# Kernel tuning notes

Measured on AMD Instinct MI355X. Metric: run time of the kernel, lower is better.

The kernel has to match this reference:

```python
import jax, jax.numpy as jnp
import numpy as np

ALPHA = 0.5            # conf['alpha'] hybrid mixing
MAX_TOP_ANT = 50       # conf['max_top_antecedents']
MAX_SPAN_WIDTH = 30


def bucket_distance(d):
    # util.bucket_distance: identity 0..4, then log2 buckets, clipped to [0, 9]
    logspace = jnp.floor(jnp.log2(jnp.maximum(d, 1).astype(jnp.float32))).astype(d.dtype) + 3
    return jnp.clip(jnp.where(d <= 4, d, logspace), 0, 9)


def setup_inputs() -> dict:
    key = jax.random.key(0)
    ks = jax.random.split(key, 16)
    W, D, K, F, H = 4096, 768, 768, 20, 1000
    SPAN = 3 * D                      # span_emb_size = 3 * bert_emb_size
    PAIR = 3 * SPAN + F               # pair_emb_size (use_features only)
    std = 0.02

    mention_doc = jax.random.normal(ks[0], (W, D), jnp.float32)
    mention_doc_one = jax.random.normal(ks[1], (W, D), jnp.float32)
    top_span_starts = jnp.sort(jax.random.randint(ks[2], (K,), 0, W - MAX_SPAN_WIDTH))
    widths = jax.random.randint(ks[3], (K,), 0, MAX_SPAN_WIDTH)
    top_span_ends = jnp.minimum(top_span_starts + widths, W - 1)
    top_span_mention_scores = jax.random.normal(ks[4], (K,), jnp.float32)

    return {
        "mention_doc": mention_doc,
        "mention_doc_one": mention_doc_one,
        "top_span_starts": top_span_starts,
        "top_span_ends": top_span_ends,
        "top_span_mention_scores": top_span_mention_scores,
        # mention_token_attn: Linear(D -> 1)
        "attn_w": jax.random.normal(ks[5], (D,), jnp.float32) * std,
        "attn_b": jnp.zeros((), jnp.float32),
        # coarse_bilinear: Linear(SPAN -> SPAN)
        "coarse_w": jax.random.normal(ks[6], (SPAN, SPAN), jnp.float32) * std,
        "coarse_b": jnp.zeros((SPAN,), jnp.float32),
        # emb_antecedent_distance_prior [10, F] + antecedent_distance_score_ffnn Linear(F -> 1)
        "dist_prior_emb": jax.random.normal(ks[7], (10, F), jnp.float32) * std,
        "dist_w": jax.random.normal(ks[8], (F,), jnp.float32) * std,
        "dist_b": jnp.zeros((), jnp.float32),
        # emb_top_antecedent_distance [10, F]
        "top_dist_emb": jax.random.normal(ks[9], (10, F), jnp.float32) * std,
        # coref_score_ffnn: Linear(PAIR -> H), ReLU, Linear(H -> 1)
        "coref_w1": jax.random.normal(ks[10], (PAIR, H), jnp.float32) * std,
        "coref_b1": jnp.zeros((H,), jnp.float32),
        "coref_w2": jax.random.normal(ks[11], (H,), jnp.float32) * std,
        "coref_b2": jnp.zeros((), jnp.float32),
    }


def reference(mention_doc, mention_doc_one, top_span_starts, top_span_ends,
              top_span_mention_scores, attn_w, attn_b, coarse_w, coarse_b,
              dist_prior_emb, dist_w, dist_b, top_dist_emb,
              coref_w1, coref_b1, coref_w2, coref_b2):
    W = mention_doc.shape[0]
    K = top_span_starts.shape[0]
    C = min(K, MAX_TOP_ANT)
    NEG_INF = jnp.float32(-1e30) * 0 - jnp.inf  # true -inf, matches torch.log(0.)

    # --- span embeddings: start / end / head-attention over hybrid doc ---
    start_emb = mention_doc[top_span_starts]                      # [K, D]
    end_emb = mention_doc[top_span_ends]                          # [K, D]
    hybrid = mention_doc * (1.0 - ALPHA) + mention_doc_one * ALPHA
    token_attn = hybrid @ attn_w + attn_b                         # [W]
    tok = jnp.arange(W)
    span_tok_mask = (tok[None, :] >= top_span_starts[:, None]) & \
                    (tok[None, :] <= top_span_ends[:, None])      # [K, W]
    attn_raw = jnp.where(span_tok_mask, token_attn[None, :], NEG_INF)
    attn_probs = jax.nn.softmax(attn_raw, axis=1)                 # [K, W]
    head_emb = attn_probs @ hybrid                                # [K, D]
    span_emb = jnp.concatenate([start_emb, end_emb, head_emb], axis=1)  # [K, 3D]

    # --- coarse (fast) pairwise scores ---
    rng = jnp.arange(K)
    ant_offsets = rng[:, None] - rng[None, :]                     # [K, K]
    ant_mask = ant_offsets >= 1
    pair_sum = top_span_mention_scores[:, None] + top_span_mention_scores[None, :]
    src = span_emb @ coarse_w + coarse_b                          # coarse_bilinear
    fast = pair_sum + src @ span_emb.T
    fast = jnp.where(ant_mask, fast, NEG_INF)                     # + log(mask)
    dist_score = dist_prior_emb @ dist_w + dist_b                 # [10]
    fast = fast + dist_score[bucket_distance(ant_offsets)]        # distance prior

    # --- top-k antecedent pruning ---
    top_fast, top_idx = jax.lax.top_k(fast, C)                    # [K, C]
    top_ant_offsets = jnp.take_along_axis(ant_offsets, top_idx, axis=1)

    # --- fine-grained pairwise FFNN scoring ---
    dist_emb = top_dist_emb[bucket_distance(top_ant_offsets)]     # [K, C, F]
    ant_emb = span_emb[top_idx]                                   # [K, C, 3D]
    tgt_emb = jnp.broadcast_to(span_emb[:, None, :], ant_emb.shape)
    sim_emb = span_emb[:, None, :] * ant_emb
    pair_emb = jnp.concatenate([tgt_emb, ant_emb, sim_emb, dist_emb], axis=-1)  # [K, C, PAIR]
    h = jax.nn.relu(jnp.einsum('kcp,ph->kch', pair_emb, coref_w1) + coref_b1)
    slow = jnp.einsum('kch,h->kc', h, coref_w2) + coref_b2        # [K, C]
    top_scores = slow + top_fast

    # dummy antecedent (epsilon) column of zeros
    return jnp.concatenate([jnp.zeros((K, 1), top_scores.dtype), top_scores], axis=1)
```

## Files before the change

kernel.cpp:

```cpp
#include <hip/hip_runtime.h>
#include <math.h>

#define WTOK 4096
#define DD   768
#define KK   768
#define SPAN 2304
#define HH   1000
#define CC   50
#define NPAD 1024
#define NBIG 4352

typedef __attribute__((ext_vector_type(8))) short bf16x8;
typedef __attribute__((ext_vector_type(4))) float f32x4;
typedef unsigned short ushort;
typedef unsigned int uint;
typedef unsigned long long u64;

__device__ __forceinline__ int bucketd(int d) {
  int l = (d >= 1) ? (31 - __clz(d)) : 0;
  int v = (d <= 4) ? d : (l + 3);
  return min(max(v, 0), 9);
}
__device__ __forceinline__ ushort f2bf(float f) {
  uint u = __float_as_uint(f);
  return (ushort)((u + 0x7fffu + ((u >> 16) & 1u)) >> 16);
}
__device__ __forceinline__ uint pkmul_t(uint a, uint b) {
  float lo = __uint_as_float(a << 16) * __uint_as_float(b << 16);
  float hi = __uint_as_float(a & 0xffff0000u) * __uint_as_float(b & 0xffff0000u);
  return __builtin_amdgcn_perm(__float_as_uint(hi), __float_as_uint(lo), 0x07060302u);
}
__device__ __forceinline__ uint4 pkmul4(uint4 a, uint4 b) {
  uint4 r;
  r.x = pkmul_t(a.x, b.x); r.y = pkmul_t(a.y, b.y);
  r.z = pkmul_t(a.z, b.z); r.w = pkmul_t(a.w, b.w);
  return r;
}
__device__ __forceinline__ void dma16(const ushort* g, ushort* l) {
  __builtin_amdgcn_global_load_lds(
      (const __attribute__((address_space(1))) void*)g,
      (__attribute__((address_space(3))) void*)l, 16, 0, 0);
}
__device__ __forceinline__ u64 shflx64(u64 v, int msk) {
  uint lo = (uint)v, hi = (uint)(v >> 32);
  lo = (uint)__shfl_xor((int)lo, msk, 64);
  hi = (uint)__shfl_xor((int)hi, msk, 64);
  return ((u64)hi << 32) | lo;
}

#define PB_COARSE 5184
#define PB_W 2304
#define PB_SETUP_BASE (PB_COARSE + 3 * PB_W)
#define PB_SLOW_BASE  (PB_SETUP_BASE + 40)
#define PB_HYB_BASE   (PB_SLOW_BASE + 150)
#define PB_TOTAL      (PB_HYB_BASE + WTOK)

__global__ __launch_bounds__(256) void prep_k(
    const float* __restrict__ coarse_w, const float* __restrict__ W1,
    const float* __restrict__ dist_prior, const float* __restrict__ dist_w,
    const float* __restrict__ dist_b, const float* __restrict__ top_dist,
    const float* __restrict__ doc, const float* __restrict__ doc1,
    const float* __restrict__ attn_w, const float* __restrict__ attn_b,
    ushort* __restrict__ BigT, ushort* __restrict__ W1simT,
    float* __restrict__ dist_score, float* __restrict__ Pdist,
    float* __restrict__ slow, float* __restrict__ hybrid,
    float* __restrict__ tok_attn)
{
  int bid = blockIdx.x;
  int tid = threadIdx.x;
  if (bid >= PB_HYB_BASE) {
    int w = bid - PB_HYB_BASE;
    float part = 0.f;
    for (int d = tid; d < DD; d += 256) {
      float h = 0.5f * doc[(long)w * DD + d] + 0.5f * doc1[(long)w * DD + d];
      hybrid[(long)w * DD + d] = h;
      part += h * attn_w[d];
    }
    for (int off = 32; off > 0; off >>= 1) part += __shfl_down(part, off, 64);
    __shared__ float ws4[4];
    if ((tid & 63) == 0) ws4[tid >> 6] = part;
    __syncthreads();
    if (tid == 0) tok_attn[w] = ws4[0] + ws4[1] + ws4[2] + ws4[3] + attn_b[0];
    return;
  }
  if (bid >= PB_SLOW_BASE) {
    int t = (bid - PB_SLOW_BASE) * 256 + tid;
    if (t < KK * CC) slow[t] = 0.f;
    return;
  }
  if (bid >= PB_SETUP_BASE) {
    int t = (bid - PB_SETUP_BASE) * 256 + tid;
    if (t < 10) {
      float s = dist_b[0];
      for (int f = 0; f < 20; ++f) s += dist_prior[t * 20 + f] * dist_w[f];
      dist_score[t] = s;
    }
    if (t < 10 * HH) {
      int b = t / HH, h = t % HH;
      float s = 0.f;
      for (int f = 0; f < 20; ++f)
        s += top_dist[b * 20 + f] * W1[(long)(6912 + f) * HH + h];
      Pdist[t] = s;
    }
    return;
  }
  const float* in; int ldin, Cin, nbase, NBrows; ushort* out; int idx;
  int xt;
  if (bid < PB_COARSE) {
    idx = bid; in = coarse_w; ldin = SPAN; Cin = SPAN; nbase = 0;
    NBrows = NBIG; out = BigT; xt = SPAN / 32;
  } else {
    idx = bid - PB_COARSE;
    int region = idx / PB_W;
    idx = idx % PB_W;
    if (region == 0) { in = W1; nbase = 2304; NBrows = NBIG; out = BigT; }
    else if (region == 1) { in = W1 + (size_t)SPAN * HH; nbase = 3328; NBrows = NBIG; out = BigT; }
    else { in = W1 + (size_t)2 * SPAN * HH; nbase = 0; NBrows = NPAD; out = W1simT; }
    ldin = HH; Cin = HH; xt = NPAD / 32;
  }
  {
    int bx = idx % xt, by = idx / xt;
    __shared__ float tile[32][33];
    int n0 = bx * 32, p0 = by * 32;
    int tx = tid & 31, ty = tid >> 5;
    for (int i = ty; i < 32; i += 8) {
      int p = p0 + i, n = n0 + tx;
      tile[i][tx] = (n < Cin) ? in[(long)p * ldin + n] : 0.f;
    }
    __syncthreads();
    size_t slab = (size_t)(p0 >> 5) * NBrows * 32;
    for (int i = ty; i < 32; i += 8) {
      int n = n0 + i;
      out[slab + (size_t)(nbase + n) * 32 + tx] = f2bf(tile[tx][i]);
    }
  }
}

__global__ __launch_bounds__(256) void span_emb_k(
    const float* __restrict__ doc, const float* __restrict__ hybrid,
    const float* __restrict__ tok_attn, const int* __restrict__ starts,
    const int* __restrict__ ends, ushort* __restrict__ se_bf)
{
  int k = blockIdx.x;
  int s = starts[k], e = ends[k];
  int len = e - s + 1;
  int tid = threadIdx.x;
  __shared__ float p_s[32];
  if (tid < 32) {
    float v = (tid < len) ? tok_attn[s + tid] : -INFINITY;
    float m = v;
    for (int msk = 16; msk >= 1; msk >>= 1) m = fmaxf(m, __shfl_xor(m, msk, 32));
    float pe = (tid < len) ? expf(v - m) : 0.f;
    float Z = pe;
    for (int msk = 16; msk >= 1; msk >>= 1) Z += __shfl_xor(Z, msk, 32);
    p_s[tid] = pe / Z;
  }
  __syncthreads();
  for (int d = tid; d < DD; d += 256) {
    float h = 0.f;
    for (int t = 0; t < len; ++t) h += p_s[t] * hybrid[(long)(s + t) * DD + d];
    se_bf[(long)k * SPAN + d]          = f2bf(doc[(long)s * DD + d]);
    se_bf[(long)k * SPAN + DD + d]     = f2bf(doc[(long)e * DD + d]);
    se_bf[(long)k * SPAN + 2 * DD + d] = f2bf(h);
  }
}

__global__ __launch_bounds__(256) void gemm_combined_k(
    const ushort* __restrict__ A, const ushort* __restrict__ B,
    const float* __restrict__ coarse_b, const float* __restrict__ b1,
    ushort* __restrict__ src_bf, float* __restrict__ Ptgt,
    float* __restrict__ Pant)
{
  __shared__ __align__(16) ushort As[2][64 * 40];
  __shared__ __align__(16) ushort Bs[2][128 * 32];
  int tid = threadIdx.x;
  int m0 = blockIdx.x * 64, n0 = blockIdx.y * 128;
  int lane = tid & 63, wid = tid >> 6;
  int quad = lane >> 4, lr = lane & 15;
  int wm = (wid & 1) << 5, wn = (wid >> 1) << 6;
  int arow = tid >> 2, aq = tid & 3;
  int gofs[2];
#pragma unroll
  for (int t = 0; t < 2; ++t) {
    int S = t * 256 + tid;
    int r = S >> 2, p = S & 3;
    int q = p ^ ((r >> 1) & 3);
    gofs[t] = (n0 + r) * 32 + q * 8;
  }
  const ushort* ga = A + (size_t)(m0 + arow) * SPAN + aq * 8;
  {
    uint4 a0 = *(const uint4*)(ga);
    dma16(B + gofs[0], &Bs[0][(size_t)(0 * 256 + tid) * 8]);
    dma16(B + gofs[1], &Bs[0][(size_t)(1 * 256 + tid) * 8]);
    *(uint4*)&As[0][arow * 40 + aq * 8] = a0;
  }
  __syncthreads();
  f32x4 acc[2][4] = {};
  for (int k0 = 0; k0 < SPAN; k0 += 32) {
    int buf = (k0 >> 5) & 1, nb = buf ^ 1;
    bool more = (k0 + 32) < SPAN;
    uint4 a_nxt;
    if (more) {
      a_nxt = *(const uint4*)(ga + k0 + 32);
      const ushort* sb = B + (size_t)((k0 >> 5) + 1) * (NBIG * 32);
      dma16(sb + gofs[0], &Bs[nb][(size_t)(0 * 256 + tid) * 8]);
      dma16(sb + gofs[1], &Bs[nb][(size_t)(1 * 256 + tid) * 8]);
    }
    bf16x8 af[2], bfr[4];
#pragma unroll
    for (int mi = 0; mi < 2; ++mi)
      af[mi] = *(const bf16x8*)&As[buf][(wm + mi * 16 + lr) * 40 + quad * 8];
#pragma unroll
    for (int ni = 0; ni < 4; ++ni) {
      int r = wn + ni * 16 + lr;
      int p = quad ^ ((r >> 1) & 3);
      bfr[ni] = *(const bf16x8*)&Bs[buf][r * 32 + p * 8];
    }
#pragma unroll
    for (int mi = 0; mi < 2; ++mi)
#pragma unroll
      for (int ni = 0; ni < 4; ++ni)
        acc[mi][ni] = __builtin_amdgcn_mfma_f32_16x16x32_bf16(
            af[mi], bfr[ni], acc[mi][ni], 0, 0, 0);
    if (more) *(uint4*)&As[nb][arow * 40 + aq * 8] = a_nxt;
    __syncthreads();
  }
#pragma unroll
  for (int mi = 0; mi < 2; ++mi)
#pragma unroll
    for (int ni = 0; ni < 4; ++ni) {
      f32x4 c = acc[mi][ni];
#pragma unroll
      for (int reg = 0; reg < 4; ++reg) {
        int gm = m0 + wm + mi * 16 + quad * 4 + reg;
        int g = n0 + wn + ni * 16 + lr;
        float v = c[reg];
        if (g < 2304) {
          src_bf[(size_t)gm * SPAN + g] = f2bf(v + coarse_b[g]);
        } else if (g < 3328) {
          int n = g - 2304;
          if (n < HH) Ptgt[(size_t)gm * HH + n] = v + b1[n];
        } else {
          int n = g - 3328;
          if (n < HH) Pant[(size_t)gm * HH + n] = v;
        }
      }
    }
}

__global__ __launch_bounds__(256) void gemm_fast_k(
    const ushort* __restrict__ A, const ushort* __restrict__ B,
    const float* __restrict__ ms, const float* __restrict__ dist_score,
    float* __restrict__ fast)
{
  __shared__ __align__(16) ushort As[2][64 * 40];
  __shared__ __align__(16) ushort Bs[2][64 * 40];
  int tid = threadIdx.x;
  int m0 = blockIdx.x * 64, n0 = blockIdx.y * 64;
  int lane = tid & 63, wid = tid >> 6;
  int quad = lane >> 4, lr = lane & 15;
  int wm = (wid & 1) << 5, wn = (wid >> 1) << 5;
  int row = tid >> 2, aq = tid & 3;
  const ushort* ga = A + (size_t)(m0 + row) * SPAN + aq * 8;
  const ushort* gb = B + (size_t)(n0 + row) * SPAN + aq * 8;
  {
    uint4 a0 = *(const uint4*)(ga);
    uint4 b0 = *(const uint4*)(gb);
    *(uint4*)&As[0][row * 40 + aq * 8] = a0;
    *(uint4*)&Bs[0][row * 40 + aq * 8] = b0;
  }
  __syncthreads();
  f32x4 acc[2][2] = {};
  for (int k0 = 0; k0 < SPAN; k0 += 32) {
    int buf = (k0 >> 5) & 1, nb = buf ^ 1;
    bool more = (k0 + 32) < SPAN;
    uint4 a_nxt, b_nxt;
    if (more) {
      a_nxt = *(const uint4*)(ga + k0 + 32);
      b_nxt = *(const uint4*)(gb + k0 + 32);
    }
    bf16x8 af[2], bfr[2];
#pragma unroll
    for (int mi = 0; mi < 2; ++mi)
      af[mi] = *(const bf16x8*)&As[buf][(wm + mi * 16 + lr) * 40 + quad * 8];
#pragma unroll
    for (int ni = 0; ni < 2; ++ni)
      bfr[ni] = *(const bf16x8*)&Bs[buf][(wn + ni * 16 + lr) * 40 + quad * 8];
#pragma unroll
    for (int mi = 0; mi < 2; ++mi)
#pragma unroll
      for (int ni = 0; ni < 2; ++ni)
        acc[mi][ni] = __builtin_amdgcn_mfma_f32_16x16x32_bf16(
            af[mi], bfr[ni], acc[mi][ni], 0, 0, 0);
    if (more) {
      *(uint4*)&As[nb][row * 40 + aq * 8] = a_nxt;
      *(uint4*)&Bs[nb][row * 40 + aq * 8] = b_nxt;
    }
    __syncthreads();
  }
#pragma unroll
  for (int mi = 0; mi < 2; ++mi)
#pragma unroll
    for (int ni = 0; ni < 2; ++ni) {
      f32x4 c = acc[mi][ni];
#pragma unroll
      for (int reg = 0; reg < 4; ++reg) {
        int gm = m0 + wm + mi * 16 + quad * 4 + reg;
        int gn = n0 + wn + ni * 16 + lr;
        float v;
        if (gn < gm) {
          v = c[reg] + ms[gm] + ms[gn] + dist_score[bucketd(gm - gn)];
        } else {
          v = -INFINITY;
        }
        fast[(size_t)gm * KK + gn] = v;
      }
    }
}

__global__ __launch_bounds__(256) void topk_k(
    const float* __restrict__ fast, float* __restrict__ top_fast,
    int* __restrict__ row_j, int* __restrict__ row_bucket)
{
  int lane = threadIdx.x & 63;
  int k = blockIdx.x * 4 + (threadIdx.x >> 6);
  u64 key[12];
#pragma unroll
  for (int i = 0; i < 12; ++i) {
    int j = lane + i * 64;
    uint u = __float_as_uint(fast[(size_t)k * KK + j]);
    uint s = (u & 0x80000000u) ? ~u : (u | 0x80000000u);
    key[i] = ((u64)s << 10) | (u64)(1023 - j);
  }
  for (int it = 0; it < CC; ++it) {
    u64 gm = key[0];
#pragma unroll
    for (int i = 1; i < 12; ++i) gm = (key[i] > gm) ? key[i] : gm;
    for (int msk = 32; msk > 0; msk >>= 1) {
      u64 o = shflx64(gm, msk);
      gm = (o > gm) ? o : gm;
    }
#pragma unroll
    for (int i = 0; i < 12; ++i) if (key[i] == gm) key[i] = 0;
    if (lane == 0) {
      uint s = (uint)(gm >> 10);
      uint u = (s & 0x80000000u) ? (s & 0x7fffffffu) : ~s;
      int j = 1023 - (int)(gm & 1023u);
      int r = k * CC + it;
      top_fast[r] = __uint_as_float(u);
      row_j[r] = j;
      row_bucket[r] = bucketd(k - j);
    }
  }
}

__global__ __launch_bounds__(512, 4) void pair_mfma_k(
    const ushort* __restrict__ se_bf, const ushort* __restrict__ W1simT,
    const int* __restrict__ row_j, const int* __restrict__ row_bucket,
    const float* __restrict__ Ptgt, const float* __restrict__ Pant,
    const float* __restrict__ Pdist, const float* __restrict__ w2,
    float* __restrict__ slow)
{
  __shared__ __align__(16) ushort As[2][128 * 32];
  __shared__ __align__(16) ushort Bs[2][256 * 32];
  __shared__ int ks_s[128];
  __shared__ int js_s[128];
  __shared__ int bk_s[128];
  int tid = threadIdx.x;
  int m0 = blockIdx.x * 128, n0 = blockIdx.y * 256;
  if (tid < 128) {
    int r = m0 + tid;
    ks_s[tid] = r / CC;
    js_s[tid] = row_j[r];
    bk_s[tid] = row_bucket[r];
  }
  __syncthreads();
  int lane = tid & 63, wid = tid >> 6;
  int quad = lane >> 4, lr = lane & 15;
  int wm = (wid & 3) << 5;
  int wn = (wid >> 2) << 7;
  int ar0 = tid >> 2, aq = tid & 3;
  const ushort* pk0 = se_bf + (size_t)ks_s[ar0] * SPAN + aq * 8;
  const ushort* pj0 = se_bf + (size_t)js_s[ar0] * SPAN + aq * 8;
  int gofs[2];
#pragma unroll
  for (int t = 0; t < 2; ++t) {
    int S = t * 512 + tid;
    int r = S >> 2, p = S & 3;
    int q = p ^ ((r >> 1) & 3);
    gofs[t] = (n0 + r) * 32 + q * 8;
  }
  int awi0 = ar0 * 32 + (aq ^ ((ar0 >> 1) & 3)) * 8;

  {
    uint4 ka0 = *(const uint4*)(pk0);
    uint4 ja0 = *(const uint4*)(pj0);
#pragma unroll
    for (int t = 0; t < 2; ++t)
      dma16(W1simT + gofs[t], &Bs[0][(size_t)(t * 512 + tid) * 8]);
    *(uint4*)&As[0][awi0] = pkmul4(ka0, ja0);
  }
  __syncthreads();

  f32x4 acc[2][8] = {};
  for (int k0 = 0; k0 < SPAN; k0 += 32) {
    int buf = (k0 >> 5) & 1, nb = buf ^ 1;
    bool more = (k0 + 32) < SPAN;
    int k1 = more ? k0 + 32 : k0;
    uint4 ka0 = *(const uint4*)(pk0 + k1);
    uint4 ja0 = *(const uint4*)(pj0 + k1);
    if (more) {
      const ushort* sb = W1simT + (size_t)(k1 >> 5) * (NPAD * 32);
#pragma unroll
      for (int t = 0; t < 2; ++t)
        dma16(sb + gofs[t], &Bs[nb][(size_t)(t * 512 + tid) * 8]);
    }
    bf16x8 af[2], bfr[8];
#pragma unroll
    for (int mi = 0; mi < 2; ++mi) {
      int r = wm + mi * 16 + lr;
      int p = quad ^ ((r >> 1) & 3);
      af[mi] = *(const bf16x8*)&As[buf][r * 32 + p * 8];
    }
#pragma unroll
    for (int ni = 0; ni < 8; ++ni) {
      int r = wn + ni * 16 + lr;
      int p = quad ^ ((r >> 1) & 3);
      bfr[ni] = *(const bf16x8*)&Bs[buf][r * 32 + p * 8];
    }
#pragma unroll
    for (int ni = 0; ni < 8; ++ni)
#pragma unroll
      for (int mi = 0; mi < 2; ++mi)
        acc[mi][ni] = __builtin_amdgcn_mfma_f32_16x16x32_bf16(
            af[mi], bfr[ni], acc[mi][ni], 0, 0, 0);
    if (more) {
      *(uint4*)&As[nb][awi0] = pkmul4(ka0, ja0);
    }
    __syncthreads();
  }
  int nn[8]; float w2r[8]; bool nv[8];
#pragma unroll
  for (int ni = 0; ni < 8; ++ni) {
    nn[ni] = n0 + wn + ni * 16 + lr;
    nv[ni] = nn[ni] < HH;
    w2r[ni] = nv[ni] ? w2[nn[ni]] : 0.f;
  }
#pragma unroll
  for (int mi = 0; mi < 2; ++mi) {
#pragma unroll
    for (int reg = 0; reg < 4; ++reg) {
      int rl = wm + mi * 16 + quad * 4 + reg;
      int kk = ks_s[rl], jj = js_s[rl], bb = bk_s[rl];
      float s = 0.f;
#pragma unroll
      for (int ni = 0; ni < 8; ++ni) {
        if (nv[ni]) {
          float h = acc[mi][ni][reg] + Ptgt[(size_t)kk * HH + nn[ni]] +
                    Pant[(size_t)jj * HH + nn[ni]] +
                    Pdist[(size_t)bb * HH + nn[ni]];
          s += fmaxf(h, 0.f) * w2r[ni];
        }
      }
      s += __shfl_xor(s, 1); s += __shfl_xor(s, 2);
      s += __shfl_xor(s, 4); s += __shfl_xor(s, 8);
      if (lr == 0) atomicAdd(&slow[m0 + rl], s);
    }
  }
}

__global__ void finalize_k(const float* __restrict__ slow,
                           const float* __restrict__ top_fast,
                           const float* __restrict__ b2, float* __restrict__ out)
{
  int t = blockIdx.x * 256 + threadIdx.x;
  if (t >= KK * (CC + 1)) return;
  int k = t / (CC + 1), col = t % (CC + 1);
  if (col == 0) {
    out[t] = 0.f;
  } else {
    int r = k * CC + col - 1;
    float v = slow[r] + b2[0] + top_fast[r];
    if (!isfinite(v)) v = -1.0e30f;
    out[t] = v;
  }
}

extern "C" void kernel_launch(void* const* d_in, const int* in_sizes, int n_in,
                              void* d_out, int out_size, void* d_ws, size_t ws_size,
                              hipStream_t stream)
{
  const float* doc        = (const float*)d_in[0];
  const float* doc1       = (const float*)d_in[1];
  const int*   starts     = (const int*)d_in[2];
  const int*   ends       = (const int*)d_in[3];
  const float* ms         = (const float*)d_in[4];
  const float* attn_w     = (const float*)d_in[5];
  const float* attn_b     = (const float*)d_in[6];
  const float* coarse_w   = (const float*)d_in[7];
  const float* coarse_b   = (const float*)d_in[8];
  const float* dist_prior = (const float*)d_in[9];
  const float* dist_w     = (const float*)d_in[10];
  const float* dist_b     = (const float*)d_in[11];
  const float* top_dist   = (const float*)d_in[12];
  const float* W1         = (const float*)d_in[13];
  const float* b1         = (const float*)d_in[14];
  const float* w2         = (const float*)d_in[15];
  const float* b2         = (const float*)d_in[16];
  float* out = (float*)d_out;

  char* ws = (char*)d_ws;
  size_t off = 0;
  auto alloc = [&](size_t bytes) { void* p = ws + off; off = (off + bytes + 1023) & ~(size_t)1023; return p; };
  float*  hybrid     = (float*)alloc((size_t)WTOK * DD * 4);
  float*  tok_attn   = (float*)alloc((size_t)WTOK * 4);
  ushort* se_bf      = (ushort*)alloc((size_t)KK * SPAN * 2 + 4096);
  ushort* src_bf     = (ushort*)alloc((size_t)KK * SPAN * 2 + 4096);
  float*  fast       = (float*)alloc((size_t)KK * KK * 4);
  float*  Ptgt       = (float*)alloc((size_t)KK * HH * 4);
  float*  Pant       = (float*)alloc((size_t)KK * HH * 4);
  float*  Pdist      = (float*)alloc((size_t)10 * HH * 4);
  float*  dist_score = (float*)alloc(64);
  float*  top_fast   = (float*)alloc((size_t)KK * CC * 4);
  int*    row_j      = (int*)alloc((size_t)KK * CC * 4);
  int*    row_bucket = (int*)alloc((size_t)KK * CC * 4);
  float*  slow       = (float*)alloc((size_t)KK * CC * 4);
  ushort* BigT       = (ushort*)alloc((size_t)NBIG * SPAN * 2 + 4096);
  ushort* W1simT     = (ushort*)alloc((size_t)NPAD * SPAN * 2 + 4096);
  (void)ws_size; (void)in_sizes; (void)n_in; (void)out_size;

  prep_k<<<PB_TOTAL, 256, 0, stream>>>(coarse_w, W1, dist_prior, dist_w,
                                       dist_b, top_dist, doc, doc1, attn_w,
                                       attn_b, BigT, W1simT, dist_score,
                                       Pdist, slow, hybrid, tok_attn);
  span_emb_k<<<KK, 256, 0, stream>>>(doc, hybrid, tok_attn, starts, ends, se_bf);
  {
    dim3 g(KK / 64, NBIG / 128);
    gemm_combined_k<<<g, 256, 0, stream>>>(se_bf, BigT, coarse_b, b1,
                                           src_bf, Ptgt, Pant);
  }
  {
    dim3 g(KK / 64, KK / 64);
    gemm_fast_k<<<g, 256, 0, stream>>>(src_bf, se_bf, ms, dist_score, fast);
  }
  topk_k<<<KK / 4, 256, 0, stream>>>(fast, top_fast, row_j, row_bucket);
  {
    dim3 g((KK * CC) / 128, NPAD / 256);
    pair_mfma_k<<<g, 512, 0, stream>>>(se_bf, W1simT, row_j, row_bucket,
                                       Ptgt, Pant, Pdist, w2, slow);
  }
  finalize_k<<<(KK * (CC + 1) + 255) / 256, 256, 0, stream>>>(slow, top_fast, b2, out);
}
```

Measured before the change: 479.3 us.

## Double K-step per iteration in GEMMs and widen weight transpose tiles to 64

Both bf16 GEMM kernels now stage 64 K-elements per pipeline stage instead of 32, which halves the number of barrier-synchronized iterations and issues more MFMAs and loads between syncs. The weight-transpose prep kernel moves from 32x32 to 64x64 tiles, so it launches fewer blocks and writes wider contiguous runs. The cost is more LDS per block, which may lower occupancy, and the transpose output indexing becomes more complex.

```diff
diff --git a/kernel.cpp b/kernel.cpp
--- a/kernel.cpp
+++ b/kernel.cpp
@@ -48,8 +48,8 @@
   return ((u64)hi << 32) | lo;
 }
 
-#define PB_COARSE 5184
-#define PB_W 2304
+#define PB_COARSE 1296
+#define PB_W 576
 #define PB_SETUP_BASE (PB_COARSE + 3 * PB_W)
 #define PB_SLOW_BASE  (PB_SETUP_BASE + 40)
 #define PB_HYB_BASE   (PB_SLOW_BASE + 150)
@@ -108,7 +108,7 @@
   int xt;
   if (bid < PB_COARSE) {
     idx = bid; in = coarse_w; ldin = SPAN; Cin = SPAN; nbase = 0;
-    NBrows = NBIG; out = BigT; xt = SPAN / 32;
+    NBrows = NBIG; out = BigT; xt = SPAN / 64;
   } else {
     idx = bid - PB_COARSE;
     int region = idx / PB_W;
@@ -116,22 +116,22 @@
     if (region == 0) { in = W1; nbase = 2304; NBrows = NBIG; out = BigT; }
     else if (region == 1) { in = W1 + (size_t)SPAN * HH; nbase = 3328; NBrows = NBIG; out = BigT; }
     else { in = W1 + (size_t)2 * SPAN * HH; nbase = 0; NBrows = NPAD; out = W1simT; }
-    ldin = HH; Cin = HH; xt = NPAD / 32;
+    ldin = HH; Cin = HH; xt = NPAD / 64;
   }
   {
     int bx = idx % xt, by = idx / xt;
-    __shared__ float tile[32][33];
-    int n0 = bx * 32, p0 = by * 32;
-    int tx = tid & 31, ty = tid >> 5;
-    for (int i = ty; i < 32; i += 8) {
+    __shared__ float tile[64][65];
+    int n0 = bx * 64, p0 = by * 64;
+    int tx = tid & 63, ty = tid >> 6;
+    for (int i = ty; i < 64; i += 4) {
       int p = p0 + i, n = n0 + tx;
       tile[i][tx] = (n < Cin) ? in[(long)p * ldin + n] : 0.f;
     }
     __syncthreads();
-    size_t slab = (size_t)(p0 >> 5) * NBrows * 32;
-    for (int i = ty; i < 32; i += 8) {
+    size_t obase = (size_t)(((p0 + tx) >> 5)) * NBrows * 32 + (tx & 31);
+    for (int i = ty; i < 64; i += 4) {
       int n = n0 + i;
-      out[slab + (size_t)(nbase + n) * 32 + tx] = f2bf(tile[tx][i]);
+      out[obase + (size_t)(nbase + n) * 32] = f2bf(tile[tx][i]);
     }
   }
 }
@@ -171,8 +171,8 @@
     ushort* __restrict__ src_bf, float* __restrict__ Ptgt,
     float* __restrict__ Pant)
 {
-  __shared__ __align__(16) ushort As[2][64 * 40];
-  __shared__ __align__(16) ushort Bs[2][128 * 32];
+  __shared__ __align__(16) ushort As[2][64 * 72];
+  __shared__ __align__(16) ushort Bs[2][2][128 * 32];
   int tid = threadIdx.x;
   int m0 = blockIdx.x * 64, n0 = blockIdx.y * 128;
   int lane = tid & 63, wid = tid >> 6;
@@ -189,40 +189,59 @@
   }
   const ushort* ga = A + (size_t)(m0 + arow) * SPAN + aq * 8;
   {
-    uint4 a0 = *(const uint4*)(ga);
-    dma16(B + gofs[0], &Bs[0][(size_t)(0 * 256 + tid) * 8]);
-    dma16(B + gofs[1], &Bs[0][(size_t)(1 * 256 + tid) * 8]);
-    *(uint4*)&As[0][arow * 40 + aq * 8] = a0;
+    uint4 alo = *(const uint4*)(ga);
+    uint4 ahi = *(const uint4*)(ga + 32);
+#pragma unroll
+    for (int kh = 0; kh < 2; ++kh)
+#pragma unroll
+      for (int t = 0; t < 2; ++t)
+        dma16(B + (size_t)kh * (NBIG * 32) + gofs[t],
+              &Bs[0][kh][(size_t)(t * 256 + tid) * 8]);
+    *(uint4*)&As[0][arow * 72 + aq * 8] = alo;
+    *(uint4*)&As[0][arow * 72 + 32 + aq * 8] = ahi;
   }
   __syncthreads();
   f32x4 acc[2][4] = {};
-  for (int k0 = 0; k0 < SPAN; k0 += 32) {
-    int buf = (k0 >> 5) & 1, nb = buf ^ 1;
-    bool more = (k0 + 32) < SPAN;
-    uint4 a_nxt;
+  for (int s = 0; s < 36; ++s) {
+    int buf = s & 1, nb = buf ^ 1;
+    bool more = (s + 1) < 36;
+    uint4 alo, ahi;
     if (more) {
-      a_nxt = *(const uint4*)(ga + k0 + 32);
-      const ushort* sb = B + (size_t)((k0 >> 5) + 1) * (NBIG * 32);
-      dma16(sb + gofs[0], &Bs[nb][(size_t)(0 * 256 + tid) * 8]);
-      dma16(sb + gofs[1], &Bs[nb][(size_t)(1 * 256 + tid) * 8]);
-    }
-    bf16x8 af[2], bfr[4];
+      alo = *(const uint4*)(ga + (s + 1) * 64);
+      ahi = *(const uint4*)(ga + (s + 1) * 64 + 32);
+#pragma unroll
+      for (int kh = 0; kh < 2; ++kh)
+#pragma unroll
+        for (int t = 0; t < 2; ++t)
+          dma16(B + (size_t)(2 * (s + 1) + kh) * (NBIG * 32) + gofs[t],
+                &Bs[nb][kh][(size_t)(t * 256 + tid) * 8]);
+    }
+    bf16x8 af[2][2], bfr[4][2];
 #pragma unroll
     for (int mi = 0; mi < 2; ++mi)
-      af[mi] = *(const bf16x8*)&As[buf][(wm + mi * 16 + lr) * 40 + quad * 8];
+#pragma unroll
+      for (int kh = 0; kh < 2; ++kh)
+        af[mi][kh] = *(const bf16x8*)&As[buf][(wm + mi * 16 + lr) * 72 + kh * 32 + quad * 8];
 #pragma unroll
     for (int ni = 0; ni < 4; ++ni) {
       int r = wn + ni * 16 + lr;
       int p = quad ^ ((r >> 1) & 3);
-      bfr[ni] = *(const bf16x8*)&Bs[buf][r * 32 + p * 8];
-    }
-#pragma unroll
-    for (int mi = 0; mi < 2; ++mi)
-#pragma unroll
-      for (int ni = 0; ni < 4; ++ni)
-        acc[mi][ni] = __builtin_amdgcn_mfma_f32_16x16x32_bf16(
-            af[mi], bfr[ni], acc[mi][ni], 0, 0, 0);
-    if (more) *(uint4*)&As[nb][arow * 40 + aq * 8] = a_nxt;
+#pragma unroll
+      for (int kh = 0; kh < 2; ++kh)
+        bfr[ni][kh] = *(const bf16x8*)&Bs[buf][kh][r * 32 + p * 8];
+    }
+#pragma unroll
+    for (int kh = 0; kh < 2; ++kh)
+#pragma unroll
+      for (int mi = 0; mi < 2; ++mi)
+#pragma unroll
+        for (int ni = 0; ni < 4; ++ni)
+          acc[mi][ni] = __builtin_amdgcn_mfma_f32_16x16x32_bf16(
+              af[mi][kh], bfr[ni][kh], acc[mi][ni], 0, 0, 0);
+    if (more) {
+      *(uint4*)&As[nb][arow * 72 + aq * 8] = alo;
+      *(uint4*)&As[nb][arow * 72 + 32 + aq * 8] = ahi;
+    }
     __syncthreads();
   }
 #pragma unroll
@@ -253,8 +272,8 @@
     const float* __restrict__ ms, const float* __restrict__ dist_score,
     float* __restrict__ fast)
 {
-  __shared__ __align__(16) ushort As[2][64 * 40];
-  __shared__ __align__(16) ushort Bs[2][64 * 40];
+  __shared__ __align__(16) ushort As[2][64 * 72];
+  __shared__ __align__(16) ushort Bs[2][64 * 72];
   int tid = threadIdx.x;
   int m0 = blockIdx.x * 64, n0 = blockIdx.y * 64;
   int lane = tid & 63, wid = tid >> 6;
@@ -265,36 +284,50 @@
   const ushort* gb = B + (size_t)(n0 + row) * SPAN + aq * 8;
   {
     uint4 a0 = *(const uint4*)(ga);
+    uint4 a1 = *(const uint4*)(ga + 32);
     uint4 b0 = *(const uint4*)(gb);
-    *(uint4*)&As[0][row * 40 + aq * 8] = a0;
-    *(uint4*)&Bs[0][row * 40 + aq * 8] = b0;
+    uint4 b1v = *(const uint4*)(gb + 32);
+    *(uint4*)&As[0][row * 72 + aq * 8] = a0;
+    *(uint4*)&As[0][row * 72 + 32 + aq * 8] = a1;
+    *(uint4*)&Bs[0][row * 72 + aq * 8] = b0;
+    *(uint4*)&Bs[0][row * 72 + 32 + aq * 8] = b1v;
   }
   __syncthreads();
   f32x4 acc[2][2] = {};
-  for (int k0 = 0; k0 < SPAN; k0 += 32) {
-    int buf = (k0 >> 5) & 1, nb = buf ^ 1;
-    bool more = (k0 + 32) < SPAN;
-    uint4 a_nxt, b_nxt;
+  for (int s = 0; s < 36; ++s) {
+    int buf = s & 1, nb = buf ^ 1;
+    bool more = (s + 1) < 36;
+    uint4 a0, a1, b0, b1v;
     if (more) {
-      a_nxt = *(const uint4*)(ga + k0 + 32);
-      b_nxt = *(const uint4*)(gb + k0 + 32);
-    }
-    bf16x8 af[2], bfr[2];
+      a0 = *(const uint4*)(ga + (s + 1) * 64);
+      a1 = *(const uint4*)(ga + (s + 1) * 64 + 32);
+      b0 = *(const uint4*)(gb + (s + 1) * 64);
+      b1v = *(const uint4*)(gb + (s + 1) * 64 + 32);
+    }
+    bf16x8 af[2][2], bfr[2][2];
 #pragma unroll
     for (int mi = 0; mi < 2; ++mi)
-      af[mi] = *(const bf16x8*)&As[buf][(wm + mi * 16 + lr) * 40 + quad * 8];
+#pragma unroll
+      for (int kh = 0; kh < 2; ++kh)
+        af[mi][kh] = *(const bf16x8*)&As[buf][(wm + mi * 16 + lr) * 72 + kh * 32 + quad * 8];
 #pragma unroll
     for (int ni = 0; ni < 2; ++ni)
-      bfr[ni] = *(const bf16x8*)&Bs[buf][(wn + ni * 16 + lr) * 40 + quad * 8];
-#pragma unroll
-    for (int mi = 0; mi < 2; ++mi)
-#pragma unroll
-      for (int ni = 0; ni < 2; ++ni)
-        acc[mi][ni] = __builtin_amdgcn_mfma_f32_16x16x32_bf16(
-            af[mi], bfr[ni], acc[mi][ni], 0, 0, 0);
+#pragma unroll
+      for (int kh = 0; kh < 2; ++kh)
+        bfr[ni][kh] = *(const bf16x8*)&Bs[buf][(wn + ni * 16 + lr) * 72 + kh * 32 + quad * 8];
+#pragma unroll
+    for (int kh = 0; kh < 2; ++kh)
+#pragma unroll
+      for (int mi = 0; mi < 2; ++mi)
+#pragma unroll
+        for (int ni = 0; ni < 2; ++ni)
+          acc[mi][ni] = __builtin_amdgcn_mfma_f32_16x16x32_bf16(
+              af[mi][kh], bfr[ni][kh], acc[mi][ni], 0, 0, 0);
     if (more) {
-      *(uint4*)&As[nb][row * 40 + aq * 8] = a_nxt;
-      *(uint4*)&Bs[nb][row * 40 + aq * 8] = b_nxt;
+      *(uint4*)&As[nb][row * 72 + aq * 8] = a0;
+      *(uint4*)&As[nb][row * 72 + 32 + aq * 8] = a1;
+      *(uint4*)&Bs[nb][row * 72 + aq * 8] = b0;
+      *(uint4*)&Bs[nb][row * 72 + 32 + aq * 8] = b1v;
     }
     __syncthreads();
   }
```

Measured after the change: 476.9 us. About the same (-0.5%).
